# Optimization experiments

Hardware: AMD Instinct MI355X
Metric: run time of the kernel (lower is better)

The kernel has to match this reference:

```python
import jax, jax.numpy as jnp
import numpy as np

K = 2  # top-k experts per token


def setup_inputs() -> dict:
    key = jax.random.key(0)
    kx, kw = jax.random.split(key)
    N, D, E = 16384, 4096, 64
    x = jax.random.normal(kx, (N, D), dtype=jnp.float32)
    # nn.Linear(input_dim, num_experts, bias=False) weight: [num_experts, input_dim]
    W = jax.random.normal(kw, (E, D), dtype=jnp.float32) * (1.0 / np.sqrt(D))
    return {"x": x, "W": W}


def reference(x, W):
    # logits = x @ W^T : [N, E]
    logits = jnp.einsum('nd,ed->ne', x, W)
    top_k_logits, top_k_indices = jax.lax.top_k(logits, K)  # [N, K]
    top_k_weights = jax.nn.softmax(top_k_logits, axis=-1)   # softmax over the k selected
    N = logits.shape[0]
    rows = jnp.arange(N)[:, None]  # [N, 1] broadcast against [N, K]
    full_weights = jnp.zeros_like(logits).at[rows, top_k_indices].set(top_k_weights)
    return full_weights, top_k_indices
```

## Files before the change

kernel.cpp:

```cpp
#include <hip/hip_runtime.h>
#include <math.h>

#define N_TOK 16384
#define DDIM  4096
#define NEXP  64
#define TM    32
#define NSL   8
#define KSL   (DDIM / NSL)
#define LSTR  68
#define TAU   1e-3f

typedef __attribute__((ext_vector_type(8))) short bf16x8;
typedef __attribute__((ext_vector_type(4))) float f32x4;

__device__ __forceinline__ void split8(f32x4 v0, f32x4 v1, bf16x8& hi, bf16x8& lo) {
    float f[8];
    *(f32x4*)&f[0] = v0;  *(f32x4*)&f[4] = v1;
    #pragma unroll
    for (int i = 0; i < 8; ++i) {
        unsigned u  = __float_as_uint(f[i]);
        unsigned uh = u & 0xFFFF0000u;
        float    rf = f[i] - __uint_as_float(uh);
        hi[i] = (short)(u >> 16);
        lo[i] = (short)(__float_as_uint(rf) >> 16);
    }
}

__global__ __launch_bounds__(1024, 8) void topk_gate_kernel(
    const float* __restrict__ x, const float* __restrict__ W,
    float* __restrict__ out)
{
    __shared__ float  Lgh[NSL][TM][LSTR];
    __shared__ int    top_i[TM * 2];
    __shared__ float  top_w[TM * 2];
    __shared__ int    nflag;
    __shared__ int    flist[TM];
    __shared__ double red[512];
    __shared__ double lgd[NEXP];
    __shared__ int    rbi[2];
    __shared__ float  rbw[2];

    const int tid  = threadIdx.x;
    const int lane = tid & 63;
    const int w    = tid >> 6;
    const int tg   = w & 1;
    const int ks   = w >> 1;
    const int block_tok = blockIdx.x * TM;

    const int r16  = lane & 15;
    const int koct = lane >> 4;

    const float* xp = x + (size_t)(block_tok + tg * 16 + r16) * DDIM
                        + ks * KSL + koct * 8;
    const float* wp0 = W + (size_t)r16 * DDIM + ks * KSL + koct * 8;

    f32x4 acc[4];
    #pragma unroll
    for (int t = 0; t < 4; ++t) acc[t] = (f32x4){0.f, 0.f, 0.f, 0.f};

    #pragma unroll 2
    for (int kb = 0; kb < KSL; kb += 32) {
        f32x4 a0 = *(const f32x4*)(xp + kb);
        f32x4 a1 = *(const f32x4*)(xp + kb + 4);
        bf16x8 ah, al;
        split8(a0, a1, ah, al);
        #pragma unroll
        for (int t = 0; t < 4; ++t) {
            const float* wp = wp0 + (size_t)t * 16 * DDIM + kb;
            f32x4 b0 = *(const f32x4*)(wp);
            f32x4 b1 = *(const f32x4*)(wp + 4);
            bf16x8 bh, bl;
            split8(b0, b1, bh, bl);
            acc[t] = __builtin_amdgcn_mfma_f32_16x16x32_bf16(ah, bh, acc[t], 0, 0, 0);
            acc[t] = __builtin_amdgcn_mfma_f32_16x16x32_bf16(ah, bl, acc[t], 0, 0, 0);
            acc[t] = __builtin_amdgcn_mfma_f32_16x16x32_bf16(al, bh, acc[t], 0, 0, 0);
        }
    }

    #pragma unroll
    for (int t = 0; t < 4; ++t)
        #pragma unroll
        for (int r = 0; r < 4; ++r)
            Lgh[ks][tg * 16 + koct * 4 + r][t * 16 + r16] = acc[t][r];
    if (tid == 0) nflag = 0;
    __syncthreads();

    if (tid < 512) {
        const int tok = tid >> 4;
        const int e4  = (tid & 15) * 4;
        float4 s = *(const float4*)&Lgh[0][tok][e4];
        #pragma unroll
        for (int h = 1; h < NSL; ++h) {
            float4 v = *(const float4*)&Lgh[h][tok][e4];
            s.x += v.x; s.y += v.y; s.z += v.z; s.w += v.w;
        }
        *(float4*)&Lgh[0][tok][e4] = s;
    }
    __syncthreads();

    if (tid < TM) {
        float m1 = -INFINITY, m2 = -INFINITY, m3 = -INFINITY;
        int i1 = 0, i2 = 0;
        for (int e = 0; e < NEXP; ++e) {
            float v = Lgh[0][tid][e];
            if (v > m1)      { m3 = m2; m2 = m1; i2 = i1; m1 = v; i1 = e; }
            else if (v > m2) { m3 = m2; m2 = v; i2 = e; }
            else if (v > m3) { m3 = v; }
        }
        float d  = expf(m2 - m1);
        float rn = 1.0f / (1.0f + d);
        top_i[tid * 2 + 0] = i1;  top_i[tid * 2 + 1] = i2;
        top_w[tid * 2 + 0] = rn;  top_w[tid * 2 + 1] = d * rn;
        float2* oi = (float2*)(out + (size_t)N_TOK * NEXP);
        oi[block_tok + tid] = make_float2((float)i1, (float)i2);
        if ((m1 - m2 < TAU) || (m2 - m3 < TAU)) {
            int p = atomicAdd(&nflag, 1);
            flist[p] = tid;
        }
    }
    __syncthreads();

    if (tid < 512) {
        float4* ow = (float4*)(out + (size_t)block_tok * NEXP);
        const int tok = tid >> 4;
        const int e4  = (tid & 15) * 4;
        int a1 = top_i[tok * 2], a2 = top_i[tok * 2 + 1];
        float v1 = top_w[tok * 2], v2 = top_w[tok * 2 + 1];
        float4 v; float* vp = (float*)&v;
        #pragma unroll
        for (int q = 0; q < 4; ++q) {
            int e = e4 + q;
            vp[q] = (e == a1) ? v1 : ((e == a2) ? v2 : 0.0f);
        }
        ow[tid] = v;
    }
    __syncthreads();

    const int fn = nflag;
    for (int f = 0; f < fn; ++f) {
        const int tok = block_tok + flist[f];
        if (tid < 512) {
            const int e = tid & 63, q = tid >> 6;
            const float* wr = W + (size_t)e * DDIM + q * (DDIM / 8);
            const float* xr = x + (size_t)tok * DDIM + q * (DDIM / 8);
            double p = 0.0;
            for (int k = 0; k < DDIM / 8; k += 4) {
                float4 wv = *(const float4*)(wr + k);
                float4 xv = *(const float4*)(xr + k);
                p += (double)xv.x * (double)wv.x;
                p += (double)xv.y * (double)wv.y;
                p += (double)xv.z * (double)wv.z;
                p += (double)xv.w * (double)wv.w;
            }
            red[tid] = p;
        }
        __syncthreads();
        if (tid < 64) {
            double s = 0.0;
            #pragma unroll
            for (int j = 0; j < 8; ++j) s += red[tid + 64 * j];
            lgd[tid] = s;
        }
        __syncthreads();

        if (tid == 0) {
            double m1 = -INFINITY, m2 = -INFINITY;
            int i1 = 0, i2 = 0;
            for (int ee = 0; ee < NEXP; ++ee) {
                double v = lgd[ee];
                if (v > m1)      { m2 = m1; i2 = i1; m1 = v; i1 = ee; }
                else if (v > m2) { m2 = v; i2 = ee; }
            }
            double d  = exp(m2 - m1);
            double rn = 1.0 / (1.0 + d);
            rbi[0] = i1; rbi[1] = i2;
            rbw[0] = (float)rn; rbw[1] = (float)(d * rn);
            float2* oi = (float2*)(out + (size_t)N_TOK * NEXP);
            oi[tok] = make_float2((float)i1, (float)i2);
        }
        __syncthreads();

        if (tid < 16) {
            float4 v = make_float4(0.f, 0.f, 0.f, 0.f);
            float* vp = (float*)&v;
            #pragma unroll
            for (int qq = 0; qq < 4; ++qq) {
                int ee = tid * 4 + qq;
                if (ee == rbi[0]) vp[qq] = rbw[0];
                else if (ee == rbi[1]) vp[qq] = rbw[1];
            }
            ((float4*)(out + (size_t)tok * NEXP))[tid] = v;
        }
        __syncthreads();
    }
}

extern "C" void kernel_launch(void* const* d_in, const int* in_sizes, int n_in,
                              void* d_out, int out_size, void* d_ws, size_t ws_size,
                              hipStream_t stream) {
    const float* x = (const float*)d_in[0];
    const float* W = (const float*)d_in[1];
    float* out = (float*)d_out;
    (void)in_sizes; (void)n_in; (void)d_ws; (void)ws_size; (void)out_size;

    hipLaunchKernelGGL(topk_gate_kernel, dim3(N_TOK / TM), dim3(1024), 0, stream,
                       x, W, out);
}
```

Baseline: 575.7 us.

## Warp-specialize x loads via global_load_lds pipeline and pre-pack W into bf16 hi/lo

Splits each 512-thread block into producer waves that stream x tiles into a 4-stage swizzled LDS ring with global_load_lds, and consumer waves that run the split-bf16 MFMAs from LDS. W is converted once per call into MFMA-ready bf16 hi/lo fragments in workspace by a separate pack kernel, so the main loop no longer splits W. Each consumer wave handles 32 tokens over a quarter of K, which cuts the cross-slice reduction. The cost is an extra kernel launch, barrier-heavy producer/consumer synchronisation, and only half the waves doing math.

```diff
diff --git a/kernel.cpp b/kernel.cpp
--- a/kernel.cpp
+++ b/kernel.cpp
@@ -5,8 +5,10 @@
 #define DDIM  4096
 #define NEXP  64
 #define TM    32
-#define NSL   8
-#define KSL   (DDIM / NSL)
+#define NQ    4
+#define KQ    (DDIM / NQ)
+#define BKQ   32
+#define NSTEP (KQ / BKQ)
 #define LSTR  68
 #define TAU   1e-3f
 
@@ -26,16 +28,41 @@
     }
 }
 
-__global__ __launch_bounds__(1024, 8) void topk_gate_kernel(
-    const float* __restrict__ x, const float* __restrict__ W,
-    float* __restrict__ out)
+__device__ __forceinline__ void gl2lds16(const void* g, void* l) {
+    __builtin_amdgcn_global_load_lds(
+        (const __attribute__((address_space(1))) unsigned int*)g,
+        (__attribute__((address_space(3))) unsigned int*)l,
+        16, 0, 0);
+}
+
+__global__ __launch_bounds__(256) void pack_w_kernel(
+    const float* __restrict__ W, short* __restrict__ Wp)
 {
-    __shared__ float  Lgh[NSL][TM][LSTR];
+    const int c    = blockIdx.x;
+    const int tid  = threadIdx.x;
+    const int t    = tid >> 6;
+    const int lane = tid & 63;
+    const int r16  = lane & 15;
+    const int koct = lane >> 4;
+    const float* src = W + (size_t)(t * 16 + r16) * DDIM + c * 32 + koct * 8;
+    f32x4 b0 = *(const f32x4*)src;
+    f32x4 b1 = *(const f32x4*)(src + 4);
+    bf16x8 hi, lo;
+    split8(b0, b1, hi, lo);
+    short* d = Wp + ((size_t)(c * 4 + t) * 2) * 512 + lane * 8;
+    *(bf16x8*)d         = hi;
+    *(bf16x8*)(d + 512) = lo;
+}
+
+__global__ __launch_bounds__(512, 4) void topk_gate_kernel(
+    const float* __restrict__ x, const short* __restrict__ Wp,
+    const float* __restrict__ W, float* __restrict__ out)
+{
+    __shared__ __align__(16) char sraw[4 * 16384];
     __shared__ int    top_i[TM * 2];
     __shared__ float  top_w[TM * 2];
     __shared__ int    nflag;
     __shared__ int    flist[TM];
-    __shared__ double red[512];
     __shared__ double lgd[NEXP];
     __shared__ int    rbi[2];
     __shared__ float  rbw[2];
@@ -43,58 +70,104 @@
     const int tid  = threadIdx.x;
     const int lane = tid & 63;
     const int w    = tid >> 6;
-    const int tg   = w & 1;
-    const int ks   = w >> 1;
     const int block_tok = blockIdx.x * TM;
 
-    const int r16  = lane & 15;
-    const int koct = lane >> 4;
-
-    const float* xp = x + (size_t)(block_tok + tg * 16 + r16) * DDIM
-                        + ks * KSL + koct * 8;
-    const float* wp0 = W + (size_t)r16 * DDIM + ks * KSL + koct * 8;
-
-    f32x4 acc[4];
-    #pragma unroll
-    for (int t = 0; t < 4; ++t) acc[t] = (f32x4){0.f, 0.f, 0.f, 0.f};
-
-    #pragma unroll 2
-    for (int kb = 0; kb < KSL; kb += 32) {
-        f32x4 a0 = *(const f32x4*)(xp + kb);
-        f32x4 a1 = *(const f32x4*)(xp + kb + 4);
-        bf16x8 ah, al;
-        split8(a0, a1, ah, al);
-        #pragma unroll
-        for (int t = 0; t < 4; ++t) {
-            const float* wp = wp0 + (size_t)t * 16 * DDIM + kb;
-            f32x4 b0 = *(const f32x4*)(wp);
-            f32x4 b1 = *(const f32x4*)(wp + 4);
-            bf16x8 bh, bl;
-            split8(b0, b1, bh, bl);
-            acc[t] = __builtin_amdgcn_mfma_f32_16x16x32_bf16(ah, bh, acc[t], 0, 0, 0);
-            acc[t] = __builtin_amdgcn_mfma_f32_16x16x32_bf16(ah, bl, acc[t], 0, 0, 0);
-            acc[t] = __builtin_amdgcn_mfma_f32_16x16x32_bf16(al, bh, acc[t], 0, 0, 0);
-        }
-    }
-
-    #pragma unroll
-    for (int t = 0; t < 4; ++t)
-        #pragma unroll
-        for (int r = 0; r < 4; ++r)
-            Lgh[ks][tg * 16 + koct * 4 + r][t * 16 + r16] = acc[t][r];
+    if (w >= 4) {
+        const int p  = w - 4;
+        const int sw = (((lane & 7) ^ (lane >> 3)) << 4);
+        const char* s0 = (const char*)x
+            + (size_t)(block_tok + (lane >> 3)) * (DDIM * 4)
+            + p * (KQ * 4)
+            + sw;
+        char* const dq = sraw + (p << 12);
+
+#define STAGE(S) do {                                                        \
+        char* _d = dq + (((S) & 3) << 14);                                   \
+        const char* _s = s0 + (size_t)(S) * (BKQ * 4);                       \
+        gl2lds16(_s,                  _d);                                   \
+        gl2lds16(_s + 8  * 16384UL,   _d + 1024);                            \
+        gl2lds16(_s + 16 * 16384UL,   _d + 2048);                            \
+        gl2lds16(_s + 24 * 16384UL,   _d + 3072);                            \
+    } while (0)
+
+        STAGE(0); STAGE(1); STAGE(2);
+        asm volatile("s_waitcnt vmcnt(8)" ::: "memory");
+        __builtin_amdgcn_s_barrier();
+        #pragma unroll 4
+        for (int s = 0; s < NSTEP - 3; ++s) {
+            STAGE(s + 3);
+            asm volatile("s_waitcnt vmcnt(8)" ::: "memory");
+            __builtin_amdgcn_s_barrier();
+        }
+        asm volatile("s_waitcnt vmcnt(4)" ::: "memory");
+        __builtin_amdgcn_s_barrier();
+        asm volatile("s_waitcnt vmcnt(0)" ::: "memory");
+        __builtin_amdgcn_s_barrier();
+        __builtin_amdgcn_s_barrier();
+#undef STAGE
+    } else {
+        const int h    = w;
+        const int r16  = lane & 15;
+        const int koct = lane >> 4;
+        const int q4   = (lane & 7) << 4;
+
+        f32x4 acc[2][4];
+        #pragma unroll
+        for (int tt = 0; tt < 2; ++tt)
+            #pragma unroll
+            for (int t = 0; t < 4; ++t) acc[tt][t] = (f32x4){0.f, 0.f, 0.f, 0.f};
+
+        __syncthreads();
+        #pragma unroll 4
+        for (int s = 0; s < NSTEP; ++s) {
+            const char* bbase = sraw + ((s & 3) << 14) + (h << 12);
+            bf16x8 ah[2], al[2];
+            #pragma unroll
+            for (int tt = 0; tt < 2; ++tt) {
+                const char* xb = bbase + ((tt * 16 + r16) << 7);
+                f32x4 a0 = *(const f32x4*)(xb + ((koct * 32)      ^ q4));
+                f32x4 a1 = *(const f32x4*)(xb + ((koct * 32 + 16) ^ q4));
+                split8(a0, a1, ah[tt], al[tt]);
+            }
+            const int cg = h * NSTEP + s;
+            #pragma unroll
+            for (int t = 0; t < 4; ++t) {
+                const short* wb = Wp + ((size_t)(cg * 4 + t) * 2) * 512 + lane * 8;
+                bf16x8 bh = *(const bf16x8*)wb;
+                bf16x8 bl = *(const bf16x8*)(wb + 512);
+                #pragma unroll
+                for (int tt = 0; tt < 2; ++tt) {
+                    acc[tt][t] = __builtin_amdgcn_mfma_f32_16x16x32_bf16(ah[tt], bh, acc[tt][t], 0, 0, 0);
+                    acc[tt][t] = __builtin_amdgcn_mfma_f32_16x16x32_bf16(ah[tt], bl, acc[tt][t], 0, 0, 0);
+                    acc[tt][t] = __builtin_amdgcn_mfma_f32_16x16x32_bf16(al[tt], bh, acc[tt][t], 0, 0, 0);
+                }
+            }
+            __syncthreads();
+        }
+        float* Lg = (float*)sraw;
+        #pragma unroll
+        for (int tt = 0; tt < 2; ++tt)
+            #pragma unroll
+            for (int t = 0; t < 4; ++t)
+                #pragma unroll
+                for (int r = 0; r < 4; ++r)
+                    Lg[(h * TM + tt * 16 + koct * 4 + r) * LSTR + t * 16 + r16] = acc[tt][t][r];
+    }
+
     if (tid == 0) nflag = 0;
     __syncthreads();
 
-    if (tid < 512) {
+    float* Lg = (float*)sraw;
+    {
         const int tok = tid >> 4;
         const int e4  = (tid & 15) * 4;
-        float4 s = *(const float4*)&Lgh[0][tok][e4];
-        #pragma unroll
-        for (int h = 1; h < NSL; ++h) {
-            float4 v = *(const float4*)&Lgh[h][tok][e4];
-            s.x += v.x; s.y += v.y; s.z += v.z; s.w += v.w;
-        }
-        *(float4*)&Lgh[0][tok][e4] = s;
+        float4 s0 = *(float4*)&Lg[(0 * TM + tok) * LSTR + e4];
+        #pragma unroll
+        for (int qq = 1; qq < 4; ++qq) {
+            float4 v = *(float4*)&Lg[(qq * TM + tok) * LSTR + e4];
+            s0.x += v.x; s0.y += v.y; s0.z += v.z; s0.w += v.w;
+        }
+        *(float4*)&Lg[tok * LSTR + e4] = s0;
     }
     __syncthreads();
 
@@ -102,7 +175,7 @@
         float m1 = -INFINITY, m2 = -INFINITY, m3 = -INFINITY;
         int i1 = 0, i2 = 0;
         for (int e = 0; e < NEXP; ++e) {
-            float v = Lgh[0][tid][e];
+            float v = Lg[tid * LSTR + e];
             if (v > m1)      { m3 = m2; m2 = m1; i2 = i1; m1 = v; i1 = e; }
             else if (v > m2) { m3 = m2; m2 = v; i2 = e; }
             else if (v > m3) { m3 = v; }
@@ -114,13 +187,13 @@
         float2* oi = (float2*)(out + (size_t)N_TOK * NEXP);
         oi[block_tok + tid] = make_float2((float)i1, (float)i2);
         if ((m1 - m2 < TAU) || (m2 - m3 < TAU)) {
-            int p = atomicAdd(&nflag, 1);
-            flist[p] = tid;
-        }
-    }
-    __syncthreads();
-
-    if (tid < 512) {
+            int pp = atomicAdd(&nflag, 1);
+            flist[pp] = tid;
+        }
+    }
+    __syncthreads();
+
+    {
         float4* ow = (float4*)(out + (size_t)block_tok * NEXP);
         const int tok = tid >> 4;
         const int e4  = (tid & 15) * 4;
@@ -136,23 +209,24 @@
     }
     __syncthreads();
 
+    double* red = (double*)(sraw + 40960);
     const int fn = nflag;
     for (int f = 0; f < fn; ++f) {
         const int tok = block_tok + flist[f];
-        if (tid < 512) {
+        {
             const int e = tid & 63, q = tid >> 6;
             const float* wr = W + (size_t)e * DDIM + q * (DDIM / 8);
             const float* xr = x + (size_t)tok * DDIM + q * (DDIM / 8);
-            double p = 0.0;
+            double pp = 0.0;
             for (int k = 0; k < DDIM / 8; k += 4) {
                 float4 wv = *(const float4*)(wr + k);
                 float4 xv = *(const float4*)(xr + k);
-                p += (double)xv.x * (double)wv.x;
-                p += (double)xv.y * (double)wv.y;
-                p += (double)xv.z * (double)wv.z;
-                p += (double)xv.w * (double)wv.w;
-            }
-            red[tid] = p;
+                pp += (double)xv.x * (double)wv.x;
+                pp += (double)xv.y * (double)wv.y;
+                pp += (double)xv.z * (double)wv.z;
+                pp += (double)xv.w * (double)wv.w;
+            }
+            red[tid] = pp;
         }
         __syncthreads();
         if (tid < 64) {
@@ -201,8 +275,10 @@
     const float* x = (const float*)d_in[0];
     const float* W = (const float*)d_in[1];
     float* out = (float*)d_out;
-    (void)in_sizes; (void)n_in; (void)d_ws; (void)ws_size; (void)out_size;
-
-    hipLaunchKernelGGL(topk_gate_kernel, dim3(N_TOK / TM), dim3(1024), 0, stream,
-                       x, W, out);
-}
+    short* Wp  = (short*)d_ws;
+    (void)in_sizes; (void)n_in; (void)ws_size; (void)out_size;
+
+    hipLaunchKernelGGL(pack_w_kernel, dim3(DDIM / 32), dim3(256), 0, stream, W, Wp);
+    hipLaunchKernelGGL(topk_gate_kernel, dim3(N_TOK / TM), dim3(512), 0, stream,
+                       x, Wp, W, out);
+}
```

Result: faster. 544.5 us (-5.4%).
